# Optimization experiments

Measured on AMD Instinct MI355X. Metric: run time of the kernel, lower is better.

The kernel has to match this reference:

```python
import jax, jax.numpy as jnp
import numpy as np

DIM = 1024
NUM_HEADS = 16
DIM_HEAD = 64
POOL = 8  # int(sqrt(agent_num=64))
SCALE = DIM_HEAD ** -0.5


def setup_inputs() -> dict:
    key = jax.random.key(0)
    k1, k2, k3, k4 = jax.random.split(key, 4)
    inner = NUM_HEADS * DIM_HEAD
    x = jax.random.normal(k1, (4, 4096, DIM), dtype=jnp.float32)
    # qkv Linear (no bias): weight stored as (in, out) so forward is x @ Wqkv
    Wqkv = jax.random.normal(k2, (DIM, 3 * inner), dtype=jnp.float32) * (DIM ** -0.5)
    Wo = jax.random.normal(k3, (inner, DIM), dtype=jnp.float32) * (inner ** -0.5)
    bo = jax.random.normal(k4, (DIM,), dtype=jnp.float32) * 0.01
    return {"x": x, "Wqkv": Wqkv, "Wo": Wo, "bo": bo}


def reference(x, Wqkv, Wo, bo):
    b, t, _ = x.shape
    h, d = NUM_HEADS, DIM_HEAD
    qkv = x @ Wqkv                                   # [b, t, 3*h*d]
    qkv = qkv.reshape(b, t, 3, h, d)                 # split (qkv h d)
    qkv = jnp.transpose(qkv, (2, 0, 3, 1, 4))        # [3, b, h, t, d]
    q, k, v = qkv[0], qkv[1], qkv[2]
    # AdaptiveAvgPool2d((POOL, d)) on [b,h,t,d]: identity on d, mean-pool t -> POOL
    # (t divisible by POOL -> exact reshape+mean)
    agent = q.reshape(b, h, POOL, t // POOL, d).mean(axis=3)  # [b, h, P, d]
    # stage 1: agents attend over keys, aggregate values
    s1 = jnp.einsum('bhid,bhjd->bhij', agent * SCALE, k)      # [b, h, P, t]
    p1 = jax.nn.softmax(s1, axis=-1)
    v_agent = jnp.einsum('bhij,bhjd->bhid', p1, v)            # [b, h, P, d]
    # stage 2: queries attend over agent tokens
    s2 = jnp.einsum('bhid,bhjd->bhij', q * SCALE, agent)      # [b, h, t, P]
    p2 = jax.nn.softmax(s2, axis=-1)
    out = jnp.einsum('bhij,bhjd->bhid', p2, v_agent)          # [b, h, t, d]
    out = jnp.transpose(out, (0, 2, 1, 3)).reshape(b, t, h * d)
    return out @ Wo + bo
```

## Files before the change

kernel.cpp:

```cpp
#include <hip/hip_runtime.h>
#include <hip/hip_bf16.h>
#include <stdint.h>

typedef __bf16 bf16;
typedef __attribute__((ext_vector_type(8))) __bf16 bf16x8;
typedef __attribute__((ext_vector_type(2))) __bf16 bf16x2;
typedef __attribute__((ext_vector_type(4))) float f32x4;

#define NH 16
#define DH 64
#define POOL 8
#define BATCH 4
#define SEQ 4096
#define DIMV 1024
#define QKV_N (3*DIMV)
#define M_TOTAL (BATCH*SEQ)
#define SCALE_F 0.125f
#define AGS_F (SCALE_F / 512.0f)
#define BH (BATCH*NH)
#define QKVSZ ((size_t)BH*SEQ*DH)
#define TCH 16
#define TCL (SEQ/TCH)
#define HP 128

#define AS1(p) ((const __attribute__((address_space(1))) void*)(p))
#define AS3(p) ((__attribute__((address_space(3))) void*)(p))

__global__ void convert_x(const float* __restrict__ in, bf16* __restrict__ out) {
  size_t i = ((size_t)blockIdx.x * 256 + threadIdx.x) * 8;
  float4 f0 = *(const float4*)(in + i);
  float4 f1 = *(const float4*)(in + i + 4);
  bf16x8 o;
  o[0] = (bf16)f0.x; o[1] = (bf16)f0.y; o[2] = (bf16)f0.z; o[3] = (bf16)f0.w;
  o[4] = (bf16)f1.x; o[5] = (bf16)f1.y; o[6] = (bf16)f1.z; o[7] = (bf16)f1.w;
  *(bf16x8*)(out + i) = o;
}

__global__ void transpose_f32_bf16(const float* __restrict__ in, bf16* __restrict__ out,
                                   int R, int C) {
  __shared__ float tile[32][33];
  int c0 = blockIdx.x * 32, r0 = blockIdx.y * 32;
  int tx = threadIdx.x & 31, ty = threadIdx.x >> 5;
  for (int i = ty; i < 32; i += 8)
    tile[i][tx] = in[(size_t)(r0 + i) * C + c0 + tx];
  __syncthreads();
  for (int i = ty; i < 32; i += 8)
    out[(size_t)(c0 + i) * R + r0 + tx] = (bf16)tile[tx][i];
}

template <int MODE>
__global__ __launch_bounds__(256)
void gemm_bt(const bf16* __restrict__ A, const bf16* __restrict__ B,
             void* __restrict__ Cv, const float* __restrict__ bias,
             float* __restrict__ agentSum, int M, int N, int K) {
  __shared__ bf16 As[128 * 32];
  __shared__ bf16 Bs[128 * 32];
  const int tid  = threadIdx.x;
  const int w    = tid >> 6;
  const int lane = tid & 63;
  const int m0 = blockIdx.y * 128, n0 = blockIdx.x * 128;
  const int wm = (w & 1) * 64, wn = (w >> 1) * 64;

  const bf16* Bb = (MODE == 2) ? (B + (size_t)(m0 >> 12) * N * K) : B;

  f32x4 acc[4][4] = {};

  const int g0  = w * 2;
  const int rig = lane >> 2;
  const int kcs = (lane & 3) ^ ((rig >> 1) & 3);
  const bf16* Ap0 = A + (size_t)(m0 + g0 * 16 + rig) * K + kcs * 8;
  const bf16* Ap1 = Ap0 + (size_t)16 * K;
  const bf16* Bp0 = Bb + (size_t)(n0 + g0 * 16 + rig) * K + kcs * 8;
  const bf16* Bp1 = Bp0 + (size_t)16 * K;
  bf16* AsW0 = As + g0 * 512;
  bf16* AsW1 = As + (g0 + 1) * 512;
  bf16* BsW0 = Bs + g0 * 512;
  bf16* BsW1 = Bs + (g0 + 1) * 512;

  for (int k0 = 0; k0 < K; k0 += 32) {
    __syncthreads();
    __builtin_amdgcn_global_load_lds(AS1(Ap0 + k0), AS3(AsW0), 16, 0, 0);
    __builtin_amdgcn_global_load_lds(AS1(Ap1 + k0), AS3(AsW1), 16, 0, 0);
    __builtin_amdgcn_global_load_lds(AS1(Bp0 + k0), AS3(BsW0), 16, 0, 0);
    __builtin_amdgcn_global_load_lds(AS1(Bp1 + k0), AS3(BsW1), 16, 0, 0);
    __syncthreads();

    bf16x8 a[4], b[4];
    const int C = lane >> 4;
#pragma unroll
    for (int i = 0; i < 4; ++i) {
      int ar = wm + i * 16 + (lane & 15);
      int sw = C ^ ((ar >> 1) & 3);
      a[i] = *(const bf16x8*)&As[ar * 32 + sw * 8];
    }
#pragma unroll
    for (int j = 0; j < 4; ++j) {
      int br = wn + j * 16 + (lane & 15);
      int sw = C ^ ((br >> 1) & 3);
      b[j] = *(const bf16x8*)&Bs[br * 32 + sw * 8];
    }
#pragma unroll
    for (int i = 0; i < 4; ++i)
#pragma unroll
      for (int j = 0; j < 4; ++j)
        acc[i][j] = __builtin_amdgcn_mfma_f32_16x16x32_bf16(a[i], b[j], acc[i][j], 0, 0, 0);
  }

  const int cr = (lane >> 4) * 4;
  const int cc = lane & 15;
#pragma unroll
  for (int i = 0; i < 4; ++i) {
#pragma unroll
    for (int j = 0; j < 4; ++j) {
      int rowb = m0 + wm + i * 16 + cr;
      if (MODE == 2) {
        float* Cp = (float*)Cv;
        int col = n0 + wn + j * 16 + cc;
        float bb = bias[col];
#pragma unroll
        for (int r = 0; r < 4; ++r)
          Cp[(size_t)(rowb + r) * N + col] = acc[i][j][r] + bb;
      } else {
        bf16* Cp = (bf16*)Cv;
        int nbase = n0 + wn + j * 16;
        int which = nbase >> 10;
        int hh    = (nbase >> 6) & 15;
        int dd    = (nbase & 63) + cc;
        int bb_   = rowb >> 12;
#pragma unroll
        for (int r = 0; r < 4; ++r) {
          int t = (rowb + r) & 4095;
          size_t addr = (size_t)which * QKVSZ +
                        ((size_t)(bb_ * NH + hh) * SEQ + t) * DH + dd;
          Cp[addr] = (bf16)acc[i][j][r];
        }
      }
    }
  }

  if (MODE == 0 && blockIdx.x < 8) {
    __shared__ float pool_red[4][16][4];
    float s[4];
#pragma unroll
    for (int j = 0; j < 4; ++j) {
      float t = 0.f;
#pragma unroll
      for (int i = 0; i < 4; ++i)
        t += acc[i][j][0] + acc[i][j][1] + acc[i][j][2] + acc[i][j][3];
      t += __shfl_xor(t, 16);
      t += __shfl_xor(t, 32);
      s[j] = t;
    }
    if (lane < 16) {
#pragma unroll
      for (int j = 0; j < 4; ++j) pool_red[w][lane][j] = s[j];
    }
    __syncthreads();
    if (tid < 128) {
      int wnH = tid >> 6, j = (tid >> 4) & 3, c2 = tid & 15;
      float v = pool_red[wnH * 2][c2][j] + pool_red[wnH * 2 + 1][c2][j];
      int nb  = n0 + wnH * 64 + j * 16;
      int hh  = (nb >> 6) & 15;
      int dd  = (nb & 63) + c2;
      int bb_ = m0 >> 12;
      int pp  = (m0 & 4095) >> 9;
      atomicAdd(&agentSum[((size_t)(bb_ * NH + hh) * POOL + pp) * DH + dd], v);
    }
  }
}

__global__ __launch_bounds__(256)
void stage1_fused(const bf16* __restrict__ k, const bf16* __restrict__ v,
                  const float* __restrict__ agentSum,
                  float* __restrict__ pm, float* __restrict__ pl,
                  float* __restrict__ pva) {
  const int tc = blockIdx.x, bh = blockIdx.y;
  const int tid = threadIdx.x;
  const int t0 = tc * TCL;

  __shared__ float agT[64][8];
  __shared__ float se[TCL][9];
  __shared__ float rm[4][8], rl[4][8];
  __shared__ float pr[4][8][64];

  for (int i = tid; i < 512; i += 256) {
    int p = i >> 6, d = i & 63;
    agT[d][p] = agentSum[(size_t)bh * 512 + i] * AGS_F;
  }
  __syncthreads();

  const bf16* krow = k + ((size_t)bh * SEQ + t0 + tid) * DH;
  float sc[8] = {};
#pragma unroll
  for (int dc = 0; dc < 8; ++dc) {
    bf16x8 k8 = *(const bf16x8*)(krow + dc * 8);
#pragma unroll
    for (int e = 0; e < 8; ++e) {
      float kv = (float)k8[e];
      int d = dc * 8 + e;
      float4 a0 = *(const float4*)&agT[d][0];
      float4 a1 = *(const float4*)&agT[d][4];
      sc[0] += a0.x * kv; sc[1] += a0.y * kv; sc[2] += a0.z * kv; sc[3] += a0.w * kv;
      sc[4] += a1.x * kv; sc[5] += a1.y * kv; sc[6] += a1.z * kv; sc[7] += a1.w * kv;
    }
  }

  float mx[8];
#pragma unroll
  for (int p = 0; p < 8; ++p) mx[p] = sc[p];
#pragma unroll
  for (int o = 32; o; o >>= 1)
#pragma unroll
    for (int p = 0; p < 8; ++p) mx[p] = fmaxf(mx[p], __shfl_xor(mx[p], o));
  if ((tid & 63) == 0)
#pragma unroll
    for (int p = 0; p < 8; ++p) rm[tid >> 6][p] = mx[p];
  __syncthreads();
  float m[8];
#pragma unroll
  for (int p = 0; p < 8; ++p)
    m[p] = fmaxf(fmaxf(rm[0][p], rm[1][p]), fmaxf(rm[2][p], rm[3][p]));

  float sl[8];
#pragma unroll
  for (int p = 0; p < 8; ++p) {
    float e = __expf(sc[p] - m[p]);
    se[tid][p] = e;
    sl[p] = e;
  }
#pragma unroll
  for (int o = 32; o; o >>= 1)
#pragma unroll
    for (int p = 0; p < 8; ++p) sl[p] += __shfl_xor(sl[p], o);
  if ((tid & 63) == 0)
#pragma unroll
    for (int p = 0; p < 8; ++p) rl[tid >> 6][p] = sl[p];
  __syncthreads();
  if (tid < 8) {
    float l = rl[0][tid] + rl[1][tid] + rl[2][tid] + rl[3][tid];
    pm[(size_t)(bh * TCH + tc) * 8 + tid] = m[tid];
    pl[(size_t)(bh * TCH + tc) * 8 + tid] = l;
  }

  const int p  = tid >> 5;
  const int dg = tid & 7;
  const int to = (tid >> 3) & 3;
  const bf16* vb = v + ((size_t)bh * SEQ + t0 + to) * DH + dg * 8;
  float a8[8] = {};
  for (int tl = to; tl < TCL; tl += 4) {
    float wgt = se[tl][p];
    bf16x8 v8 = *(const bf16x8*)(vb + (size_t)(tl - to) * DH);
#pragma unroll
    for (int e = 0; e < 8; ++e) a8[e] += wgt * (float)v8[e];
  }
#pragma unroll
  for (int e = 0; e < 8; ++e) pr[to][p][dg * 8 + e] = a8[e];
  __syncthreads();
  if (to == 0) {
    float* o = pva + ((size_t)(bh * TCH + tc) * 8 + p) * DH + dg * 8;
#pragma unroll
    for (int e = 0; e < 8; ++e)
      o[e] = pr[0][p][dg * 8 + e] + pr[1][p][dg * 8 + e] +
             pr[2][p][dg * 8 + e] + pr[3][p][dg * 8 + e];
  }
}

__global__ void combine_vag(const float* __restrict__ pm, const float* __restrict__ pl,
                            const float* __restrict__ pva, float* __restrict__ vag) {
  int bh = blockIdx.x;
#pragma unroll
  for (int e = threadIdx.x; e < 512; e += 256) {
    int p = e >> 6, d = e & 63;
    float M = -1e30f;
#pragma unroll
    for (int tc = 0; tc < TCH; ++tc)
      M = fmaxf(M, pm[(size_t)(bh * TCH + tc) * 8 + p]);
    float L = 0.f, acc = 0.f;
#pragma unroll
    for (int tc = 0; tc < TCH; ++tc) {
      float w = __expf(pm[(size_t)(bh * TCH + tc) * 8 + p] - M);
      L   += w * pl[(size_t)(bh * TCH + tc) * 8 + p];
      acc += w * pva[((size_t)(bh * TCH + tc) * 8 + p) * DH + d];
    }
    vag[(size_t)bh * 512 + e] = acc / L;
  }
}

__global__ void w2_build(const float* __restrict__ vag, const bf16* __restrict__ WoT,
                         bf16* __restrict__ W2T) {
  int b = blockIdx.y;
  int n = blockIdx.x * 16 + (threadIdx.x & 15);
  int h = threadIdx.x >> 4;
  __shared__ float vg[128][65];
  for (int i = threadIdx.x; i < 128 * 64; i += 256)
    vg[i >> 6][i & 63] = vag[(size_t)b * 128 * 64 + i];
  __syncthreads();
  float acc[8] = {};
  const bf16* wrow = WoT + (size_t)n * DIMV + h * 64;
#pragma unroll
  for (int dv = 0; dv < 8; ++dv) {
    bf16x8 wv = *(const bf16x8*)(wrow + dv * 8);
#pragma unroll
    for (int e = 0; e < 8; ++e) {
      float wf = (float)wv[e];
      int d = dv * 8 + e;
#pragma unroll
      for (int p = 0; p < 8; ++p) acc[p] += vg[h * 8 + p][d] * wf;
    }
  }
  bf16x8 o;
#pragma unroll
  for (int p = 0; p < 8; ++p) o[p] = (bf16)acc[p];
  *(bf16x8*)&W2T[((size_t)b * DIMV + n) * HP + h * 8] = o;
}

__global__ __launch_bounds__(256)
void p2_build(const bf16* __restrict__ q, const float* __restrict__ agentSum,
              bf16* __restrict__ P2) {
  const int bh = blockIdx.y;
  const int t  = blockIdx.x * 256 + threadIdx.x;
  const int tid = threadIdx.x;

  __shared__ float agT[64][8];
  for (int i = tid; i < 512; i += 256) {
    int p = i >> 6, d = i & 63;
    agT[d][p] = agentSum[(size_t)bh * 512 + i] * AGS_F;
  }
  __syncthreads();

  const bf16* qrow = q + ((size_t)bh * SEQ + t) * DH;
  float sc[8] = {};
#pragma unroll
  for (int dc = 0; dc < 8; ++dc) {
    bf16x8 q8 = *(const bf16x8*)(qrow + dc * 8);
#pragma unroll
    for (int e = 0; e < 8; ++e) {
      float qv = (float)q8[e];
      int d = dc * 8 + e;
      float4 a0 = *(const float4*)&agT[d][0];
      float4 a1 = *(const float4*)&agT[d][4];
      sc[0] += a0.x * qv; sc[1] += a0.y * qv; sc[2] += a0.z * qv; sc[3] += a0.w * qv;
      sc[4] += a1.x * qv; sc[5] += a1.y * qv; sc[6] += a1.z * qv; sc[7] += a1.w * qv;
    }
  }
  float m = sc[0];
#pragma unroll
  for (int p = 1; p < 8; ++p) m = fmaxf(m, sc[p]);
  float wsum = 0.f, wgt[8];
#pragma unroll
  for (int p = 0; p < 8; ++p) { wgt[p] = __expf(sc[p] - m); wsum += wgt[p]; }
  float inv = 1.0f / wsum;
  int b = bh >> 4, h = bh & 15;
  bf16x8 o8;
#pragma unroll
  for (int p = 0; p < 8; ++p) o8[p] = (bf16)(wgt[p] * inv);
  *(bf16x8*)&P2[((size_t)(b * SEQ + t)) * HP + h * 8] = o8;
}

extern "C" void kernel_launch(void* const* d_in, const int* in_sizes, int n_in,
                              void* d_out, int out_size, void* d_ws, size_t ws_size,
                              hipStream_t stream) {
  const float* x    = (const float*)d_in[0];
  const float* Wqkv = (const float*)d_in[1];
  const float* Wo   = (const float*)d_in[2];
  const float* bo   = (const float*)d_in[3];
  float* out = (float*)d_out;

  char* ws = (char*)d_ws;
  bf16* WqkvT = (bf16*)ws;                                   ws += (size_t)QKV_N * DIMV * 2;
  bf16* WoT   = (bf16*)ws;                                   ws += (size_t)DIMV * DIMV * 2;
  bf16* qkv   = (bf16*)ws;                                   ws += 3 * QKVSZ * 2;
  char* wsu   = ws;                                          ws += (size_t)M_TOTAL * DIMV * 2;
  bf16*  xb    = (bf16*)wsu;
  bf16*  P2    = (bf16*)wsu;
  bf16*  W2T   = (bf16*)(wsu + (size_t)M_TOTAL * HP * 2);
  float* agent = (float*)ws;                                 ws += 512 * 64 * 4;
  float* pm    = (float*)ws;                                 ws += BH * TCH * 8 * 4;
  float* pl    = (float*)ws;                                 ws += BH * TCH * 8 * 4;
  float* pva   = (float*)ws;                                 ws += (size_t)BH * TCH * 8 * DH * 4;
  float* vag   = (float*)ws;                                 ws += 512 * 64 * 4;

  const bf16* qp = qkv;
  const bf16* kp = qkv + QKVSZ;
  const bf16* vp = qkv + 2 * QKVSZ;

  hipMemsetAsync(agent, 0, 512 * 64 * 4, stream);

  convert_x<<<(size_t)M_TOTAL * DIMV / (256 * 8), 256, 0, stream>>>(x, xb);
  transpose_f32_bf16<<<dim3(QKV_N / 32, DIMV / 32), 256, 0, stream>>>(Wqkv, WqkvT, DIMV, QKV_N);
  transpose_f32_bf16<<<dim3(DIMV / 32, DIMV / 32), 256, 0, stream>>>(Wo, WoT, DIMV, DIMV);

  gemm_bt<0><<<dim3(QKV_N / 128, M_TOTAL / 128), 256, 0, stream>>>(
      xb, WqkvT, (void*)qkv, nullptr, agent, M_TOTAL, QKV_N, DIMV);

  p2_build<<<dim3(SEQ / 256, BH), 256, 0, stream>>>(qp, agent, P2);
  stage1_fused<<<dim3(TCH, BH), 256, 0, stream>>>(kp, vp, agent, pm, pl, pva);
  combine_vag<<<BH, 256, 0, stream>>>(pm, pl, pva, vag);
  w2_build<<<dim3(DIMV / 16, BATCH), 256, 0, stream>>>(vag, WoT, W2T);

  gemm_bt<2><<<dim3(DIMV / 128, M_TOTAL / 128), 256, 0, stream>>>(
      P2, W2T, (void*)out, bo, nullptr, M_TOTAL, DIMV, HP);
}
```

Before: 356.7 us.

## Replace QKV projection GEMM with 256x256 tiled, LDS-pipelined 8-wave kernel

Adds a dedicated QKV GEMM kernel that uses 256x256 output tiles with 512 threads, direct global-to-LDS loads (global_load_lds), XOR-swizzled LDS layout, double-buffered K stages interleaved with MFMA quadrants, and a grouped block-index swizzle for L2 locality. The agent pooling sum is now done per wave with atomics in the new epilogue, and the old pooling code is removed from the generic GEMM. The aim is more data reuse per tile and overlap of memory loads with MFMA work in the dominant GEMM, at the cost of more registers and LDS per block, more atomics, and hand-scheduled barriers that are fragile.

```diff
diff --git a/kernel.cpp b/kernel.cpp
--- a/kernel.cpp
+++ b/kernel.cpp
@@ -6,6 +6,7 @@
 typedef __attribute__((ext_vector_type(8))) __bf16 bf16x8;
 typedef __attribute__((ext_vector_type(2))) __bf16 bf16x2;
 typedef __attribute__((ext_vector_type(4))) float f32x4;
+typedef __attribute__((ext_vector_type(4))) unsigned int u32x4;
 
 #define NH 16
 #define DH 64
@@ -25,6 +26,7 @@
 
 #define AS1(p) ((const __attribute__((address_space(1))) void*)(p))
 #define AS3(p) ((__attribute__((address_space(3))) void*)(p))
+typedef const __attribute__((address_space(3))) char* lds_cp;
 
 __global__ void convert_x(const float* __restrict__ in, bf16* __restrict__ out) {
   size_t i = ((size_t)blockIdx.x * 256 + threadIdx.x) * 8;
@@ -46,6 +48,195 @@
   __syncthreads();
   for (int i = ty; i < 32; i += 8)
     out[(size_t)(c0 + i) * R + r0 + tx] = (bf16)tile[tx][i];
+}
+
+__global__ __launch_bounds__(512, 2)
+void gemm1_qkv(const bf16* __restrict__ A, const bf16* __restrict__ B,
+               bf16* __restrict__ qkvOut, float* __restrict__ agentSum) {
+  constexpr int K1 = DIMV;
+  constexpr int NI = K1 / 128;
+
+  __shared__ __align__(16) bf16 LA[2][2][8192];
+  __shared__ __align__(16) bf16 LB[2][2][8192];
+
+  const int tid  = threadIdx.x;
+  const int w    = tid >> 6;
+  const int lane = tid & 63;
+  const int wm = (w >> 2) * 128;
+  const int wn = (w & 3) * 64;
+
+  const int bid = blockIdx.x;
+  const int swz = (bid & 7) * 96 + (bid >> 3);
+  const int m0 = (swz / 12) * 256;
+  const int n0 = (swz % 12) * 256;
+
+  const int rT  = tid >> 3;
+  const int csT = (((tid & 7) ^ (rT & 7)) << 3);
+  const bf16* Ag = A + (size_t)(m0 + rT) * K1 + csT;
+  const bf16* Bg = B + (size_t)(n0 + rT) * K1 + csT;
+
+  const int rA = lane & 15, C = lane >> 4, xr = rA & 7;
+  const unsigned s0 = (unsigned)(((0 * 4 + C) ^ xr) << 4);
+  const unsigned s1 = (unsigned)(((1 * 4 + C) ^ xr) << 4);
+  const unsigned aoff = (unsigned)((wm + rA) << 7);
+  const unsigned boff = (unsigned)((wn + rA) << 7);
+
+  f32x4 acc[8][4] = {};
+  u32x4 aR[4][2], bR[4][2];
+
+#define STG(arr, Gp, half, kofs) do {                                         \
+    const bf16* _s = (Gp) + (size_t)((half) * 128) * K1 + (kofs);             \
+    char* _d = (char*)&arr[half][0] + (w << 10);                              \
+    __builtin_amdgcn_global_load_lds(AS1(_s), AS3(_d), 16, 0, 0);             \
+    __builtin_amdgcn_global_load_lds(AS1(_s + 64 * K1), AS3(_d + 8192), 16, 0, 0); \
+  } while (0)
+
+#define DSR0(d, p)    asm volatile("ds_read_b128 %0, %1" : "=v"(d) : "v"(p))
+#define DSR(d, p, o)  asm volatile("ds_read_b128 %0, %1 offset:" o : "=v"(d) : "v"(p))
+
+#define READS_A(LAb, qm) do {                                                 \
+    lds_cp _p0 = (lds_cp)(const char*)&LAb[0][0] + aoff + s0 + (qm) * 8192;   \
+    lds_cp _p1 = (lds_cp)(const char*)&LAb[0][0] + aoff + s1 + (qm) * 8192;   \
+    DSR0(aR[0][0], _p0); DSR(aR[1][0], _p0, "2048");                          \
+    DSR(aR[2][0], _p0, "4096"); DSR(aR[3][0], _p0, "6144");                   \
+    DSR0(aR[0][1], _p1); DSR(aR[1][1], _p1, "2048");                          \
+    DSR(aR[2][1], _p1, "4096"); DSR(aR[3][1], _p1, "6144");                   \
+  } while (0)
+
+#define READS_B01(LBb) do {                                                   \
+    lds_cp _p0 = (lds_cp)(const char*)&LBb[0][0] + boff + s0;                 \
+    lds_cp _p1 = (lds_cp)(const char*)&LBb[0][0] + boff + s1;                 \
+    DSR0(bR[0][0], _p0); DSR(bR[1][0], _p0, "2048");                          \
+    DSR0(bR[0][1], _p1); DSR(bR[1][1], _p1, "2048");                          \
+  } while (0)
+
+#define READS_B23(LBb) do {                                                   \
+    lds_cp _p0 = (lds_cp)(const char*)&LBb[0][0] + boff + s0;                 \
+    lds_cp _p1 = (lds_cp)(const char*)&LBb[0][0] + boff + s1;                 \
+    DSR(bR[2][0], _p0, "4096"); DSR(bR[3][0], _p0, "6144");                   \
+    DSR(bR[2][1], _p1, "4096"); DSR(bR[3][1], _p1, "6144");                   \
+  } while (0)
+
+#define MFMA_Q(qm, qn) do {                                                   \
+    asm volatile("s_waitcnt lgkmcnt(0)");                                     \
+    __builtin_amdgcn_sched_barrier(0);                                        \
+    __builtin_amdgcn_s_setprio(1);                                            \
+    _Pragma("unroll")                                                         \
+    for (int il = 0; il < 4; ++il)                                            \
+      _Pragma("unroll")                                                       \
+      for (int jj = 0; jj < 2; ++jj) {                                        \
+        f32x4& ac = acc[(qm) * 4 + il][(qn) * 2 + jj];                        \
+        ac = __builtin_amdgcn_mfma_f32_16x16x32_bf16(                         \
+            __builtin_bit_cast(bf16x8, aR[il][0]),                            \
+            __builtin_bit_cast(bf16x8, bR[(qn) * 2 + jj][0]), ac, 0, 0, 0);   \
+        ac = __builtin_amdgcn_mfma_f32_16x16x32_bf16(                         \
+            __builtin_bit_cast(bf16x8, aR[il][1]),                            \
+            __builtin_bit_cast(bf16x8, bR[(qn) * 2 + jj][1]), ac, 0, 0, 0);   \
+      }                                                                       \
+    __builtin_amdgcn_s_setprio(0);                                            \
+    __builtin_amdgcn_sched_barrier(0);                                        \
+  } while (0)
+
+#define BAR __builtin_amdgcn_s_barrier()
+
+  STG(LA[0], Ag, 0, 0); STG(LA[0], Ag, 1, 0);
+  STG(LB[0], Bg, 0, 0); STG(LB[0], Bg, 1, 0);
+  STG(LB[1], Bg, 0, 64); STG(LB[1], Bg, 1, 64);
+  asm volatile("s_waitcnt vmcnt(4)");
+  __builtin_amdgcn_sched_barrier(0);
+  BAR;
+
+  int kk = 0;
+  for (int i = 0; i < NI - 1; ++i, kk += 128) {
+    READS_A(LA[0], 0); READS_B01(LB[0]);
+    STG(LA[1], Ag, 0, kk + 64);
+    BAR; MFMA_Q(0, 0); BAR;
+    READS_B23(LB[0]);
+    STG(LA[1], Ag, 1, kk + 64);
+    BAR; MFMA_Q(0, 1); BAR;
+    READS_A(LA[0], 1);
+    STG(LB[0], Bg, 0, kk + 128);
+    BAR; MFMA_Q(1, 0); BAR;
+    STG(LB[0], Bg, 1, kk + 128);
+    BAR; MFMA_Q(1, 1);
+    asm volatile("s_waitcnt vmcnt(4)");
+    __builtin_amdgcn_sched_barrier(0);
+    BAR;
+    READS_A(LA[1], 0); READS_B01(LB[1]);
+    STG(LA[0], Ag, 0, kk + 128);
+    BAR; MFMA_Q(0, 0); BAR;
+    READS_B23(LB[1]);
+    STG(LA[0], Ag, 1, kk + 128);
+    BAR; MFMA_Q(0, 1); BAR;
+    READS_A(LA[1], 1);
+    STG(LB[1], Bg, 0, kk + 192);
+    BAR; MFMA_Q(1, 0); BAR;
+    STG(LB[1], Bg, 1, kk + 192);
+    BAR; MFMA_Q(1, 1);
+    asm volatile("s_waitcnt vmcnt(4)");
+    __builtin_amdgcn_sched_barrier(0);
+    BAR;
+  }
+  READS_A(LA[0], 0); READS_B01(LB[0]);
+  STG(LA[1], Ag, 0, kk + 64);
+  BAR; MFMA_Q(0, 0); BAR;
+  READS_B23(LB[0]);
+  STG(LA[1], Ag, 1, kk + 64);
+  BAR; MFMA_Q(0, 1); BAR;
+  READS_A(LA[0], 1);
+  BAR; MFMA_Q(1, 0); BAR;
+  MFMA_Q(1, 1);
+  asm volatile("s_waitcnt vmcnt(0)");
+  __builtin_amdgcn_sched_barrier(0);
+  BAR;
+  READS_A(LA[1], 0); READS_B01(LB[1]);
+  BAR; MFMA_Q(0, 0); BAR;
+  READS_B23(LB[1]);
+  BAR; MFMA_Q(0, 1); BAR;
+  READS_A(LA[1], 1);
+  BAR; MFMA_Q(1, 0); BAR;
+  MFMA_Q(1, 1);
+
+#undef STG
+#undef DSR0
+#undef DSR
+#undef READS_A
+#undef READS_B01
+#undef READS_B23
+#undef MFMA_Q
+#undef BAR
+
+  const int cr = (lane >> 4) * 4;
+  const int cc = lane & 15;
+  const int ncol  = n0 + wn;
+  const int which = ncol >> 10;
+  const int hh    = (ncol >> 6) & 15;
+  const int rowb  = m0 + wm;
+  const int bb_   = rowb >> 12;
+  const int tb    = rowb & 4095;
+  bf16* Cp = qkvOut + (size_t)which * QKVSZ + (size_t)(bb_ * NH + hh) * SEQ * DH;
+#pragma unroll
+  for (int i = 0; i < 8; ++i)
+#pragma unroll
+    for (int j = 0; j < 4; ++j)
+#pragma unroll
+      for (int r = 0; r < 4; ++r)
+        Cp[(size_t)(tb + i * 16 + cr + r) * DH + j * 16 + cc] = (bf16)acc[i][j][r];
+
+  if (which == 0) {
+    const int pp = tb >> 9;
+    float* ag = agentSum + ((size_t)(bb_ * NH + hh) * POOL + pp) * DH;
+#pragma unroll
+    for (int j = 0; j < 4; ++j) {
+      float s = 0.f;
+#pragma unroll
+      for (int i = 0; i < 8; ++i)
+        s += acc[i][j][0] + acc[i][j][1] + acc[i][j][2] + acc[i][j][3];
+      s += __shfl_xor(s, 16);
+      s += __shfl_xor(s, 32);
+      if (lane < 16) atomicAdd(&ag[j * 16 + lane], s);
+    }
+  }
 }
 
 template <int MODE>
@@ -135,36 +326,6 @@
           Cp[addr] = (bf16)acc[i][j][r];
         }
       }
-    }
-  }
-
-  if (MODE == 0 && blockIdx.x < 8) {
-    __shared__ float pool_red[4][16][4];
-    float s[4];
-#pragma unroll
-    for (int j = 0; j < 4; ++j) {
-      float t = 0.f;
-#pragma unroll
-      for (int i = 0; i < 4; ++i)
-        t += acc[i][j][0] + acc[i][j][1] + acc[i][j][2] + acc[i][j][3];
-      t += __shfl_xor(t, 16);
-      t += __shfl_xor(t, 32);
-      s[j] = t;
-    }
-    if (lane < 16) {
-#pragma unroll
-      for (int j = 0; j < 4; ++j) pool_red[w][lane][j] = s[j];
-    }
-    __syncthreads();
-    if (tid < 128) {
-      int wnH = tid >> 6, j = (tid >> 4) & 3, c2 = tid & 15;
-      float v = pool_red[wnH * 2][c2][j] + pool_red[wnH * 2 + 1][c2][j];
-      int nb  = n0 + wnH * 64 + j * 16;
-      int hh  = (nb >> 6) & 15;
-      int dd  = (nb & 63) + c2;
-      int bb_ = m0 >> 12;
-      int pp  = (m0 & 4095) >> 9;
-      atomicAdd(&agentSum[((size_t)(bb_ * NH + hh) * POOL + pp) * DH + dd], v);
     }
   }
 }
@@ -390,8 +551,7 @@
   transpose_f32_bf16<<<dim3(QKV_N / 32, DIMV / 32), 256, 0, stream>>>(Wqkv, WqkvT, DIMV, QKV_N);
   transpose_f32_bf16<<<dim3(DIMV / 32, DIMV / 32), 256, 0, stream>>>(Wo, WoT, DIMV, DIMV);
 
-  gemm_bt<0><<<dim3(QKV_N / 128, M_TOTAL / 128), 256, 0, stream>>>(
-      xb, WqkvT, (void*)qkv, nullptr, agent, M_TOTAL, QKV_N, DIMV);
+  gemm1_qkv<<<768, 512, 0, stream>>>(xb, WqkvT, qkv, agent);
 
   p2_build<<<dim3(SEQ / 256, BH), 256, 0, stream>>>(qp, agent, P2);
   stage1_fused<<<dim3(TCH, BH), 256, 0, stream>>>(kp, vp, agent, pm, pl, pva);
```

New measurement: 317.4 us. 11.0% less time.
